# Kernel optimization log

Hardware: AMD Instinct MI355X
Metric: run time of the kernel (lower is better)

The kernel has to match this reference:

```python
import jax, jax.numpy as jnp
import numpy as np

NP, NA = 60000, 30000          # paper / author node counts
EC, EW, EB = 300000, 150000, 150000
IN_F, HID, H, D, NCLS = 1024, 512, 4, 128, 153  # HID = H*D


def setup_inputs() -> dict:
    key = jax.random.key(0)
    ks = jax.random.split(key, 24)
    inp = {
        "x_paper": jax.random.normal(ks[0], (NP, IN_F), jnp.float32),
        "x_author": jax.random.normal(ks[1], (NA, IN_F), jnp.float32),
        "cites_src": jax.random.randint(ks[2], (EC,), 0, NP, jnp.int32),
        "cites_dst": jax.random.randint(ks[3], (EC,), 0, NP, jnp.int32),
        "writes_src": jax.random.randint(ks[4], (EW,), 0, NA, jnp.int32),
        "writes_dst": jax.random.randint(ks[5], (EW,), 0, NP, jnp.int32),
        "wb_src": jax.random.randint(ks[6], (EB,), 0, NP, jnp.int32),
        "wb_dst": jax.random.randint(ks[7], (EB,), 0, NA, jnp.int32),
        "W0": jax.random.normal(ks[8], (3, IN_F, HID), jnp.float32) * 0.02,
        "al0": jax.random.normal(ks[9], (3, H, D), jnp.float32) * 0.1,
        "ar0": jax.random.normal(ks[10], (3, H, D), jnp.float32) * 0.1,
        "W1": jax.random.normal(ks[11], (3, HID, HID), jnp.float32) * 0.03,
        "al1": jax.random.normal(ks[12], (3, H, D), jnp.float32) * 0.1,
        "ar1": jax.random.normal(ks[13], (3, H, D), jnp.float32) * 0.1,
        "W2": jax.random.normal(ks[14], (3, HID, HID), jnp.float32) * 0.03,
        "al2": jax.random.normal(ks[15], (3, H, D), jnp.float32) * 0.1,
        "ar2": jax.random.normal(ks[16], (3, H, D), jnp.float32) * 0.1,
        "linW": jax.random.normal(ks[17], (HID, NCLS), jnp.float32) * 0.02,
        "linb": jnp.zeros((NCLS,), jnp.float32),
    }
    return inp


def gat_conv(h_src, h_dst, src, dst, W, al, ar, n_dst):
    """DGL-style GATConv on one edge type (bipartite block, shared fc)."""
    zs = (h_src @ W).reshape(-1, H, D)            # (Ns,H,D)
    zd = (h_dst @ W).reshape(-1, H, D)            # (Nd,H,D)
    el = jnp.sum(zs * al, axis=-1)                # (Ns,H)
    er = jnp.sum(zd * ar, axis=-1)                # (Nd,H)
    e = jax.nn.leaky_relu(el[src] + er[dst], 0.2)  # (E,H)
    # edge softmax over incoming edges per destination node
    m = jax.ops.segment_max(e, dst, num_segments=n_dst)
    m = jnp.where(jnp.isfinite(m), m, 0.0)
    ee = jnp.exp(e - m[dst])
    s = jax.ops.segment_sum(ee, dst, num_segments=n_dst)
    a = ee / (s[dst] + 1e-9)                      # (E,H)
    # weighted message aggregation: (Nd,H,D)
    return jax.ops.segment_sum(a[:, :, None] * zs[src], dst, num_segments=n_dst)


def reference(x_paper, x_author, cites_src, cites_dst, writes_src, writes_dst,
              wb_src, wb_dst, W0, al0, ar0, W1, al1, ar1, W2, al2, ar2,
              linW, linb):
    def hetero_layer(hp, ha, W, al, ar, act):
        # HeteroGraphConv: sum-aggregate per destination node type
        op = (gat_conv(hp, hp, cites_src, cites_dst, W[0], al[0], ar[0], NP)
              + gat_conv(ha, hp, writes_src, writes_dst, W[1], al[1], ar[1], NP))
        oa = gat_conv(hp, ha, wb_src, wb_dst, W[2], al[2], ar[2], NA)
        op = op.reshape(NP, H * D)   # head-flatten as in forward()
        oa = oa.reshape(NA, H * D)
        if act:
            op, oa = jax.nn.relu(op), jax.nn.relu(oa)
        return op, oa

    hp, ha = x_paper, x_author
    hp, ha = hetero_layer(hp, ha, W0, al0, ar0, True)
    hp, ha = hetero_layer(hp, ha, W1, al1, ar1, True)
    hp, ha = hetero_layer(hp, ha, W2, al2, ar2, False)  # last layer: no activation
    return hp @ linW + linb
```

## Files before the change

kernel.cpp:

```cpp
#include <hip/hip_runtime.h>
#include <cstddef>
#include <cstdint>

static constexpr int NP = 60000, NA = 30000;
static constexpr int EC = 300000, EW = 150000, EB = 150000;
static constexpr int IN_F = 1024, HID = 512, H = 4, D = 128, NCLS = 153;
static constexpr int MPAD_P = 60032;
static constexpr int MPAD_A = 30080;

typedef __attribute__((ext_vector_type(8))) short short8;
typedef __attribute__((ext_vector_type(4))) float float4v;

__device__ __forceinline__ unsigned short f2bf(float f) {
    unsigned int u = __float_as_uint(f);
    unsigned int r = u + 0x7FFFu + ((u >> 16) & 1u);
    return (unsigned short)(r >> 16);
}
__device__ __forceinline__ float bf2f(unsigned short h) {
    return __uint_as_float(((unsigned int)h) << 16);
}

__device__ __forceinline__ void gll16(const unsigned short* g, unsigned short* l) {
    __builtin_amdgcn_global_load_lds(
        (const __attribute__((address_space(1))) unsigned int*)g,
        (__attribute__((address_space(3))) unsigned int*)l, 16, 0, 0);
}

__global__ void hist_kernel(const int* __restrict__ dst, int E, int* __restrict__ counts) {
    int e = blockIdx.x * 256 + threadIdx.x;
    if (e < E) atomicAdd(&counts[dst[e]], 1);
}

__global__ void exscan_kernel(const int* __restrict__ in, int* __restrict__ out, int n) {
    __shared__ int wsum[4];
    int t = threadIdx.x;
    int lane = t & 63, w = t >> 6;
    int carry = 0;
    const int CH = 256 * 8;
    for (int base = 0; base < n; base += CH) {
        int v[8], run[8];
        int i0 = base + t * 8;
        int tsum = 0;
#pragma unroll
        for (int j = 0; j < 8; ++j) {
            int i = i0 + j;
            v[j] = (i < n) ? in[i] : 0;
            tsum += v[j];
            run[j] = tsum;
        }
        int x = tsum;
#pragma unroll
        for (int off = 1; off < 64; off <<= 1) {
            int y = __shfl_up(x, off);
            if (lane >= off) x += y;
        }
        if (lane == 63) wsum[w] = x;
        __syncthreads();
        int wpre = 0;
        for (int ww = 0; ww < w; ++ww) wpre += wsum[ww];
        int chunktot = wsum[0] + wsum[1] + wsum[2] + wsum[3];
        int pre = carry + wpre + (x - tsum);
#pragma unroll
        for (int j = 0; j < 8; ++j) {
            int i = i0 + j;
            if (i < n) out[i] = pre + run[j] - v[j];
        }
        carry += chunktot;
        __syncthreads();
    }
    if (t == 0) out[n] = carry;
}

__global__ void fill_kernel(const int* __restrict__ src, const int* __restrict__ dst, int E,
                            int* __restrict__ cursor, int* __restrict__ col) {
    int e = blockIdx.x * 256 + threadIdx.x;
    if (e < E) {
        int pos = atomicAdd(&cursor[dst[e]], 1);
        col[pos] = src[e];
    }
}

__global__ void decomp4_kernel(const float4* __restrict__ x, ushort4* __restrict__ hi,
                               ushort4* __restrict__ lo, int M, int K, int Mpad) {
    size_t i4 = (size_t)blockIdx.x * 256 + threadIdx.x;
    size_t tot = ((size_t)Mpad * K) >> 2;
    if (i4 >= tot) return;
    size_t row = (i4 * 4) / (size_t)K;
    float4 v = make_float4(0.f, 0.f, 0.f, 0.f);
    if (row < (size_t)M) v = x[i4];
    ushort4 h, l;
    h.x = f2bf(v.x); h.y = f2bf(v.y); h.z = f2bf(v.z); h.w = f2bf(v.w);
    l.x = f2bf(v.x - bf2f(h.x)); l.y = f2bf(v.y - bf2f(h.y));
    l.z = f2bf(v.z - bf2f(h.z)); l.w = f2bf(v.w - bf2f(h.w));
    hi[i4] = h; lo[i4] = l;
}

__global__ void btprep_kernel(const float* __restrict__ W, unsigned short* __restrict__ hi,
                              unsigned short* __restrict__ lo, int K, int N, int Npad) {
    int i = blockIdx.x * 256 + threadIdx.x;
    if (i >= Npad * K) return;
    int n = i / K, k = i - n * K;
    float v = (n < N) ? W[(size_t)k * N + n] : 0.f;
    unsigned short h = f2bf(v);
    hi[i] = h;
    lo[i] = f2bf(v - bf2f(h));
}

__global__ __launch_bounds__(256, 2) void gemm_mfma3(
    const unsigned short* __restrict__ Ahi, const unsigned short* __restrict__ Alo,
    const unsigned short* __restrict__ Bhi, const unsigned short* __restrict__ Blo,
    const float* __restrict__ bias, float* __restrict__ C,
    int M, int K, int Nstore, int ldc) {
    __shared__ unsigned short Ash[128 * 32];
    __shared__ unsigned short Asl[128 * 32];
    __shared__ unsigned short Bsh[256 * 32];
    __shared__ unsigned short Bsl[256 * 32];
    int tid = threadIdx.x;
    int lane = tid & 63, w = tid >> 6;
    int wr = w >> 1, wc = w & 1;
    int bm = blockIdx.y * 128, bn = blockIdx.x * 256;
    int sr = lane >> 2;
    int sc = (lane & 3) * 8;

    float4v acc[4][8];
    float4v zf = {0.f, 0.f, 0.f, 0.f};
#pragma unroll
    for (int i = 0; i < 4; ++i)
#pragma unroll
        for (int j = 0; j < 8; ++j) acc[i][j] = zf;

    int arow = wr * 64 + (lane & 15);
    int brow = wc * 128 + (lane & 15);
    int koff = (lane >> 4) * 8;

    for (int kk = 0; kk < K; kk += 32) {
        size_t a0 = (size_t)(bm + w * 16 + sr) * K + kk + sc;
        size_t a1 = (size_t)(bm + (w + 4) * 16 + sr) * K + kk + sc;
        gll16(Ahi + a0, &Ash[w * 512]);
        gll16(Ahi + a1, &Ash[(w + 4) * 512]);
        gll16(Alo + a0, &Asl[w * 512]);
        gll16(Alo + a1, &Asl[(w + 4) * 512]);
#pragma unroll
        for (int c = 0; c < 4; ++c) {
            size_t b0 = (size_t)(bn + (w + 4 * c) * 16 + sr) * K + kk + sc;
            gll16(Bhi + b0, &Bsh[(w + 4 * c) * 512]);
            gll16(Blo + b0, &Bsl[(w + 4 * c) * 512]);
        }
        __syncthreads();
        short8 fa[4], fb[8], fl[4];
#pragma unroll
        for (int i = 0; i < 4; ++i)
            fa[i] = *(const short8*)&Ash[(arow + i * 16) * 32 + koff];
#pragma unroll
        for (int j = 0; j < 8; ++j)
            fb[j] = *(const short8*)&Bsh[(brow + j * 16) * 32 + koff];
#pragma unroll
        for (int i = 0; i < 4; ++i)
#pragma unroll
            for (int j = 0; j < 8; ++j)
                acc[i][j] = __builtin_amdgcn_mfma_f32_16x16x32_bf16(fa[i], fb[j], acc[i][j], 0, 0, 0);
#pragma unroll
        for (int i = 0; i < 4; ++i)
            fl[i] = *(const short8*)&Asl[(arow + i * 16) * 32 + koff];
#pragma unroll
        for (int i = 0; i < 4; ++i)
#pragma unroll
            for (int j = 0; j < 8; ++j)
                acc[i][j] = __builtin_amdgcn_mfma_f32_16x16x32_bf16(fl[i], fb[j], acc[i][j], 0, 0, 0);
#pragma unroll
        for (int j = 0; j < 8; ++j)
            fb[j] = *(const short8*)&Bsl[(brow + j * 16) * 32 + koff];
#pragma unroll
        for (int i = 0; i < 4; ++i)
#pragma unroll
            for (int j = 0; j < 8; ++j)
                acc[i][j] = __builtin_amdgcn_mfma_f32_16x16x32_bf16(fa[i], fb[j], acc[i][j], 0, 0, 0);
        __syncthreads();
    }
    int col0 = bn + wc * 128 + (lane & 15);
    int row00 = bm + wr * 64 + (lane >> 4) * 4;
#pragma unroll
    for (int i = 0; i < 4; ++i) {
#pragma unroll
        for (int j = 0; j < 8; ++j) {
            int col = col0 + j * 16;
            if (col >= Nstore) continue;
            float badd = bias ? bias[col] : 0.f;
            int rowb = row00 + i * 16;
#pragma unroll
            for (int r = 0; r < 4; ++r) {
                int row = rowb + r;
                if (row < M) C[(size_t)row * ldc + col] = acc[i][j][r] + badd;
            }
        }
    }
}

__global__ __launch_bounds__(256) void eler_kernel(
    const float* __restrict__ z, const float* __restrict__ al, const float* __restrict__ ar,
    float* __restrict__ el, float* __restrict__ er, int M) {
    int row = blockIdx.x * 4 + (threadIdx.x >> 6);
    int lane = threadIdx.x & 63;
    if (row >= M) return;
    const float4* zr = (const float4*)(z + (size_t)row * 512 + lane * 8);
    float4 z0 = zr[0], z1 = zr[1];
    const float4* alp = (const float4*)(al + lane * 8);
    float4 a0 = alp[0], a1 = alp[1];
    float s = z0.x * a0.x + z0.y * a0.y + z0.z * a0.z + z0.w * a0.w
            + z1.x * a1.x + z1.y * a1.y + z1.z * a1.z + z1.w * a1.w;
    s += __shfl_xor(s, 8); s += __shfl_xor(s, 4); s += __shfl_xor(s, 2); s += __shfl_xor(s, 1);
    int h = lane >> 4;
    if ((lane & 15) == 0) el[(size_t)row * 4 + h] = s;
    if (er) {
        const float4* arp = (const float4*)(ar + lane * 8);
        float4 b0 = arp[0], b1 = arp[1];
        float t = z0.x * b0.x + z0.y * b0.y + z0.z * b0.z + z0.w * b0.w
                + z1.x * b1.x + z1.y * b1.y + z1.z * b1.z + z1.w * b1.w;
        t += __shfl_xor(t, 8); t += __shfl_xor(t, 4); t += __shfl_xor(t, 2); t += __shfl_xor(t, 1);
        if ((lane & 15) == 0) er[(size_t)row * 4 + h] = t;
    }
}

__global__ void fold_kernel(const float* __restrict__ W, const float* __restrict__ ar,
                            float* __restrict__ v, int K) {
    int i = blockIdx.x * 256 + threadIdx.x;
    if (i >= K * 4) return;
    int k = i >> 2, h = i & 3;
    const float* wr = W + (size_t)k * 512 + h * 128;
    const float* a = ar + h * 128;
    float s = 0.f;
#pragma unroll 4
    for (int d = 0; d < 128; ++d) s += wr[d] * a[d];
    v[i] = s;
}

__global__ __launch_bounds__(256) void skinny_kernel(
    const float* __restrict__ h, const float* __restrict__ v,
    float* __restrict__ er, int M, int K) {
    __shared__ float vs[4096];
    for (int i = threadIdx.x; i < K * 4; i += 256) vs[i] = v[i];
    __syncthreads();
    int row = blockIdx.x * 4 + (threadIdx.x >> 6);
    int lane = threadIdx.x & 63;
    if (row >= M) return;
    const float* hr = h + (size_t)row * K;
    float a0 = 0, a1 = 0, a2 = 0, a3 = 0;
    for (int k = lane; k < K; k += 64) {
        float x = hr[k];
        float4 vv = *(const float4*)&vs[k * 4];
        a0 += x * vv.x; a1 += x * vv.y; a2 += x * vv.z; a3 += x * vv.w;
    }
#pragma unroll
    for (int off = 32; off; off >>= 1) {
        a0 += __shfl_xor(a0, off); a1 += __shfl_xor(a1, off);
        a2 += __shfl_xor(a2, off); a3 += __shfl_xor(a3, off);
    }
    if (lane == 0) *(float4*)&er[(size_t)row * 4] = make_float4(a0, a1, a2, a3);
}

__global__ __launch_bounds__(256) void agg_fused(
    const int* __restrict__ rp1, const int* __restrict__ col1, const float* __restrict__ z1,
    const float* __restrict__ el1, const float* __restrict__ er1,
    const int* __restrict__ rp2, const int* __restrict__ col2, const float* __restrict__ z2,
    const float* __restrict__ el2, const float* __restrict__ er2,
    float* __restrict__ out, unsigned short* __restrict__ hi, unsigned short* __restrict__ lo,
    int N, int do_relu) {
    int j = blockIdx.x * 4 + (threadIdx.x >> 6);
    int lane = threadIdx.x & 63;
    if (j >= N) return;
    int h = lane >> 4;
    float4 acc0 = make_float4(0, 0, 0, 0), acc1 = make_float4(0, 0, 0, 0);

    {
        int e0 = rp1[j], e1 = rp1[j + 1];
        float erh = er1[(size_t)j * 4 + h];
        float m = -INFINITY, s = 0.f;
        for (int e = e0; e < e1; ++e) {
            float x = el1[(size_t)col1[e] * 4 + h] + erh;
            x = (x >= 0.f) ? x : 0.2f * x;
            float mn = fmaxf(m, x);
            s = s * expf(m - mn) + expf(x - mn);
            m = mn;
        }
        float inv = 1.0f / (s + 1e-9f);
        for (int e = e0; e < e1; ++e) {
            int src = col1[e];
            float x = el1[(size_t)src * 4 + h] + erh;
            x = (x >= 0.f) ? x : 0.2f * x;
            float wgt = expf(x - m) * inv;
            const float4* zr = (const float4*)(z1 + (size_t)src * 512 + lane * 8);
            float4 za = zr[0], zb = zr[1];
            acc0.x += wgt * za.x; acc0.y += wgt * za.y; acc0.z += wgt * za.z; acc0.w += wgt * za.w;
            acc1.x += wgt * zb.x; acc1.y += wgt * zb.y; acc1.z += wgt * zb.z; acc1.w += wgt * zb.w;
        }
    }
    if (rp2) {
        int e0 = rp2[j], e1 = rp2[j + 1];
        float erh = er2[(size_t)j * 4 + h];
        float m = -INFINITY, s = 0.f;
        for (int e = e0; e < e1; ++e) {
            float x = el2[(size_t)col2[e] * 4 + h] + erh;
            x = (x >= 0.f) ? x : 0.2f * x;
            float mn = fmaxf(m, x);
            s = s * expf(m - mn) + expf(x - mn);
            m = mn;
        }
        float inv = 1.0f / (s + 1e-9f);
        for (int e = e0; e < e1; ++e) {
            int src = col2[e];
            float x = el2[(size_t)src * 4 + h] + erh;
            x = (x >= 0.f) ? x : 0.2f * x;
            float wgt = expf(x - m) * inv;
            const float4* zr = (const float4*)(z2 + (size_t)src * 512 + lane * 8);
            float4 za = zr[0], zb = zr[1];
            acc0.x += wgt * za.x; acc0.y += wgt * za.y; acc0.z += wgt * za.z; acc0.w += wgt * za.w;
            acc1.x += wgt * zb.x; acc1.y += wgt * zb.y; acc1.z += wgt * zb.z; acc1.w += wgt * zb.w;
        }
    }
    if (do_relu) {
        acc0.x = fmaxf(acc0.x, 0.f); acc0.y = fmaxf(acc0.y, 0.f);
        acc0.z = fmaxf(acc0.z, 0.f); acc0.w = fmaxf(acc0.w, 0.f);
        acc1.x = fmaxf(acc1.x, 0.f); acc1.y = fmaxf(acc1.y, 0.f);
        acc1.z = fmaxf(acc1.z, 0.f); acc1.w = fmaxf(acc1.w, 0.f);
    }
    float* op = out + (size_t)j * 512 + lane * 8;
    *(float4*)op = acc0;
    *(float4*)(op + 4) = acc1;
    if (hi) {
        size_t base = (size_t)j * 512 + lane * 8;
        ushort4 h0, h1, l0, l1;
        h0.x = f2bf(acc0.x); h0.y = f2bf(acc0.y); h0.z = f2bf(acc0.z); h0.w = f2bf(acc0.w);
        h1.x = f2bf(acc1.x); h1.y = f2bf(acc1.y); h1.z = f2bf(acc1.z); h1.w = f2bf(acc1.w);
        l0.x = f2bf(acc0.x - bf2f(h0.x)); l0.y = f2bf(acc0.y - bf2f(h0.y));
        l0.z = f2bf(acc0.z - bf2f(h0.z)); l0.w = f2bf(acc0.w - bf2f(h0.w));
        l1.x = f2bf(acc1.x - bf2f(h1.x)); l1.y = f2bf(acc1.y - bf2f(h1.y));
        l1.z = f2bf(acc1.z - bf2f(h1.z)); l1.w = f2bf(acc1.w - bf2f(h1.w));
        *(ushort4*)(hi + base) = h0;
        *(ushort4*)(hi + base + 4) = h1;
        *(ushort4*)(lo + base) = l0;
        *(ushort4*)(lo + base + 4) = l1;
    }
}

extern "C" void kernel_launch(void* const* d_in, const int* in_sizes, int n_in,
                              void* d_out, int out_size, void* d_ws, size_t ws_size,
                              hipStream_t stream) {
    const float* x_paper = (const float*)d_in[0];
    const float* x_author = (const float*)d_in[1];
    const int* cites_src = (const int*)d_in[2];
    const int* cites_dst = (const int*)d_in[3];
    const int* writes_src = (const int*)d_in[4];
    const int* writes_dst = (const int*)d_in[5];
    const int* wb_src = (const int*)d_in[6];
    const int* wb_dst = (const int*)d_in[7];
    const float* W0 = (const float*)d_in[8];
    const float* al0 = (const float*)d_in[9];
    const float* ar0 = (const float*)d_in[10];
    const float* W1 = (const float*)d_in[11];
    const float* al1 = (const float*)d_in[12];
    const float* ar1 = (const float*)d_in[13];
    const float* W2 = (const float*)d_in[14];
    const float* al2 = (const float*)d_in[15];
    const float* ar2 = (const float*)d_in[16];
    const float* linW = (const float*)d_in[17];
    const float* linb = (const float*)d_in[18];
    float* out = (float*)d_out;

    char* p = (char*)d_ws;
    auto alloc = [&](size_t n) { char* r = p; p += (n + 255) & ~(size_t)255; return r; };

    float* hpA = (float*)alloc((size_t)NP * 512 * 4);
    float* hpB = (float*)alloc((size_t)NP * 512 * 4);
    float* haA = (float*)alloc((size_t)NA * 512 * 4);
    float* haB = (float*)alloc((size_t)NA * 512 * 4);
    float* zbuf = (float*)alloc((size_t)NP * 512 * 4);
    float* elA = (float*)alloc((size_t)NP * 16);
    float* erA = (float*)alloc((size_t)NP * 16);
    float* elB = (float*)alloc((size_t)NP * 16);
    float* erB = (float*)alloc((size_t)NP * 16);
    float* vfold = (float*)alloc(4096 * 4);
    int* rp_c = (int*)alloc((NP + 1) * 4);
    int* col_c = (int*)alloc((size_t)EC * 4);
    int* rp_w = (int*)alloc((NP + 1) * 4);
    int* col_w = (int*)alloc((size_t)EW * 4);
    int* rp_b = (int*)alloc((NA + 1) * 4);
    int* col_b = (int*)alloc((size_t)EB * 4);
    int* cursor = (int*)alloc((NP + 1) * 4);
    int* counts = (int*)alloc((size_t)NP * 4);

    unsigned short* AhiP = (unsigned short*)alloc((size_t)MPAD_P * 1024 * 2);
    unsigned short* AloP = (unsigned short*)alloc((size_t)MPAD_P * 1024 * 2);
    unsigned short* AhiA = (unsigned short*)alloc((size_t)MPAD_A * 1024 * 2);
    unsigned short* AloA = (unsigned short*)alloc((size_t)MPAD_A * 1024 * 2);
    const int Ks[3] = {IN_F, HID, HID};
    unsigned short *bthi[3][3], *btlo[3][3];
    for (int l = 0; l < 3; ++l)
        for (int t = 0; t < 3; ++t) {
            bthi[l][t] = (unsigned short*)alloc((size_t)512 * Ks[l] * 2);
            btlo[l][t] = (unsigned short*)alloc((size_t)512 * Ks[l] * 2);
        }
    unsigned short* btLhi = (unsigned short*)alloc((size_t)256 * 512 * 2);
    unsigned short* btLlo = (unsigned short*)alloc((size_t)256 * 512 * 2);
    (void)ws_size;

    struct EdgeT { const int* src; const int* dst; int E; int n; int* rp; int* col; };
    EdgeT ets[3] = {
        {cites_src, cites_dst, EC, NP, rp_c, col_c},
        {writes_src, writes_dst, EW, NP, rp_w, col_w},
        {wb_src, wb_dst, EB, NA, rp_b, col_b},
    };
    for (int t = 0; t < 3; ++t) {
        hipMemsetAsync(counts, 0, (size_t)ets[t].n * 4, stream);
        hist_kernel<<<(ets[t].E + 255) / 256, 256, 0, stream>>>(ets[t].dst, ets[t].E, counts);
        exscan_kernel<<<1, 256, 0, stream>>>(counts, ets[t].rp, ets[t].n);
        hipMemcpyAsync(cursor, ets[t].rp, (size_t)ets[t].n * 4, hipMemcpyDeviceToDevice, stream);
        fill_kernel<<<(ets[t].E + 255) / 256, 256, 0, stream>>>(ets[t].src, ets[t].dst, ets[t].E, cursor, ets[t].col);
    }

    const float* Wl[3] = {W0, W1, W2};
    const float* alL[3] = {al0, al1, al2};
    const float* arL[3] = {ar0, ar1, ar2};

    for (int l = 0; l < 3; ++l) {
        int K = Ks[l];
        for (int t = 0; t < 3; ++t)
            btprep_kernel<<<(512 * K + 255) / 256, 256, 0, stream>>>(
                Wl[l] + (size_t)t * K * 512, bthi[l][t], btlo[l][t], K, 512, 512);
    }
    btprep_kernel<<<(256 * 512 + 255) / 256, 256, 0, stream>>>(linW, btLhi, btLlo, 512, NCLS, 256);

    decomp4_kernel<<<((size_t)MPAD_P * 1024 / 4 + 255) / 256, 256, 0, stream>>>(
        (const float4*)x_paper, (ushort4*)AhiP, (ushort4*)AloP, NP, 1024, MPAD_P);
    decomp4_kernel<<<((size_t)MPAD_A * 1024 / 4 + 255) / 256, 256, 0, stream>>>(
        (const float4*)x_author, (ushort4*)AhiA, (ushort4*)AloA, NA, 1024, MPAD_A);

    auto gemm = [&](const unsigned short* Ah, const unsigned short* Al,
                    const unsigned short* Bh, const unsigned short* Bl,
                    const float* bias, float* C, int M, int Mpad, int K, int gx,
                    int Nstore, int ldc) {
        dim3 g(gx, Mpad / 128);
        gemm_mfma3<<<g, 256, 0, stream>>>(Ah, Al, Bh, Bl, bias, C, M, K, Nstore, ldc);
    };

    const float* hp = x_paper;
    const float* ha = x_author;
    for (int l = 0; l < 3; ++l) {
        int K = Ks[l];
        float* hp_n = (l & 1) ? hpB : hpA;
        float* ha_n = (l & 1) ? haB : haA;
        float* zbuf_w = ha_n;
        const float* W = Wl[l];
        const float* al = alL[l];
        const float* ar = arL[l];
        size_t wstride = (size_t)K * 512;
        int relu = (l < 2) ? 1 : 0;

        gemm(AhiP, AloP, bthi[l][0], btlo[l][0], nullptr, zbuf, NP, MPAD_P, K, 2, 512, 512);
        gemm(AhiA, AloA, bthi[l][1], btlo[l][1], nullptr, zbuf_w, NA, MPAD_A, K, 2, 512, 512);
        eler_kernel<<<(NP + 3) / 4, 256, 0, stream>>>(zbuf, al, ar, elA, erA, NP);
        eler_kernel<<<(NA + 3) / 4, 256, 0, stream>>>(zbuf_w, al + 512, nullptr, elB, nullptr, NA);
        fold_kernel<<<(K * 4 + 255) / 256, 256, 0, stream>>>(W + wstride, ar + 512, vfold, K);
        skinny_kernel<<<(NP + 3) / 4, 256, 0, stream>>>(hp, vfold, erB, NP, K);
        agg_fused<<<(NP + 3) / 4, 256, 0, stream>>>(
            rp_c, col_c, zbuf, elA, erA,
            rp_w, col_w, zbuf_w, elB, erB,
            hp_n, nullptr, nullptr, NP, relu);
        gemm(AhiP, AloP, bthi[l][2], btlo[l][2], nullptr, zbuf, NP, MPAD_P, K, 2, 512, 512);
        decomp4_kernel<<<((size_t)MPAD_P * 512 / 4 + 255) / 256, 256, 0, stream>>>(
            (const float4*)hp_n, (ushort4*)AhiP, (ushort4*)AloP, NP, 512, MPAD_P);
        eler_kernel<<<(NP + 3) / 4, 256, 0, stream>>>(zbuf, al + 1024, nullptr, elA, nullptr, NP);
        fold_kernel<<<(K * 4 + 255) / 256, 256, 0, stream>>>(W + 2 * wstride, ar + 1024, vfold, K);
        skinny_kernel<<<(NA + 3) / 4, 256, 0, stream>>>(ha, vfold, erA, NA, K);
        agg_fused<<<(NA + 3) / 4, 256, 0, stream>>>(
            rp_b, col_b, zbuf, elA, erA,
            nullptr, nullptr, nullptr, nullptr, nullptr,
            ha_n, (l < 2) ? AhiA : nullptr, (l < 2) ? AloA : nullptr, NA, relu);
        hp = hp_n;
        ha = ha_n;
    }
    gemm(AhiP, AloP, btLhi, btLlo, linb, out, NP, MPAD_P, 512, 1, NCLS, NCLS);
}
```

Measured before the change: 3.373 ms.

## Replace split-bf16 GEMM with 256x256 tile, 4-stage LDS ring pipeline

The split-bf16 GEMM moves to a 512-thread block with a 256x256 output tile. Each of the three hi/lo product passes becomes its own stage in a 4-slot LDS ring (128KB dynamic shared memory). Global-to-LDS loads are prefetched three stages ahead and gated by vmcnt waits and raw barriers, with an XOR swizzle to cut LDS bank conflicts and setprio around the MFMA bursts. The aim is to overlap memory loads with MFMA and raise arithmetic intensity per block. In exchange it needs larger M padding, far more LDS per block (which limits occupancy), and correctness depends on the hand-counted waitcnt values.

```diff
diff --git a/kernel.cpp b/kernel.cpp
--- a/kernel.cpp
+++ b/kernel.cpp
@@ -5,8 +5,8 @@
 static constexpr int NP = 60000, NA = 30000;
 static constexpr int EC = 300000, EW = 150000, EB = 150000;
 static constexpr int IN_F = 1024, HID = 512, H = 4, D = 128, NCLS = 153;
-static constexpr int MPAD_P = 60032;
-static constexpr int MPAD_A = 30080;
+static constexpr int MPAD_P = 60160;
+static constexpr int MPAD_A = 30208;
 
 typedef __attribute__((ext_vector_type(8))) short short8;
 typedef __attribute__((ext_vector_type(4))) float float4v;
@@ -106,91 +106,128 @@
     lo[i] = f2bf(v - bf2f(h));
 }
 
-__global__ __launch_bounds__(256, 2) void gemm_mfma3(
+__global__ __launch_bounds__(512, 2) void gemm_ring(
     const unsigned short* __restrict__ Ahi, const unsigned short* __restrict__ Alo,
     const unsigned short* __restrict__ Bhi, const unsigned short* __restrict__ Blo,
     const float* __restrict__ bias, float* __restrict__ C,
     int M, int K, int Nstore, int ldc) {
-    __shared__ unsigned short Ash[128 * 32];
-    __shared__ unsigned short Asl[128 * 32];
-    __shared__ unsigned short Bsh[256 * 32];
-    __shared__ unsigned short Bsl[256 * 32];
-    int tid = threadIdx.x;
-    int lane = tid & 63, w = tid >> 6;
-    int wr = w >> 1, wc = w & 1;
-    int bm = blockIdx.y * 128, bn = blockIdx.x * 256;
-    int sr = lane >> 2;
-    int sc = (lane & 3) * 8;
-
-    float4v acc[4][8];
+    extern __shared__ unsigned short lds[];
+    const int tid = threadIdx.x;
+    const int lane = tid & 63;
+    const int w = tid >> 6;
+    const int wr = w >> 2, wc = w & 3;
+    const int bm = blockIdx.y * 256, bn = blockIdx.x * 256;
+
+    const int st_row = w * 16 + (lane >> 2);
+    const int st_sc = (((lane & 3) ^ ((lane >> 3) & 3)) << 3);
+    const size_t aoff0 = (size_t)(bm + st_row) * K + st_sc;
+    const size_t aoff1 = aoff0 + (size_t)128 * K;
+    const size_t boff0 = (size_t)(bn + st_row) * K + st_sc;
+    const size_t boff1 = boff0 + (size_t)128 * K;
+    const int ldsA = w * 512;
+    const int ldsB = 8192 + w * 512;
+
+    const int arow = wr * 128 + (lane & 15);
+    const int brow = wc * 64 + (lane & 15);
+    const int rq = ((((lane >> 4) & 3) ^ ((lane >> 1) & 3)) << 3);
+    const int aRead = arow * 32 + rq;
+    const int bRead = 8192 + brow * 32 + rq;
+
+    float4v acc[8][4];
     float4v zf = {0.f, 0.f, 0.f, 0.f};
 #pragma unroll
-    for (int i = 0; i < 4; ++i)
-#pragma unroll
-        for (int j = 0; j < 8; ++j) acc[i][j] = zf;
-
-    int arow = wr * 64 + (lane & 15);
-    int brow = wc * 128 + (lane & 15);
-    int koff = (lane >> 4) * 8;
-
-    for (int kk = 0; kk < K; kk += 32) {
-        size_t a0 = (size_t)(bm + w * 16 + sr) * K + kk + sc;
-        size_t a1 = (size_t)(bm + (w + 4) * 16 + sr) * K + kk + sc;
-        gll16(Ahi + a0, &Ash[w * 512]);
-        gll16(Ahi + a1, &Ash[(w + 4) * 512]);
-        gll16(Alo + a0, &Asl[w * 512]);
-        gll16(Alo + a1, &Asl[(w + 4) * 512]);
-#pragma unroll
-        for (int c = 0; c < 4; ++c) {
-            size_t b0 = (size_t)(bn + (w + 4 * c) * 16 + sr) * K + kk + sc;
-            gll16(Bhi + b0, &Bsh[(w + 4 * c) * 512]);
-            gll16(Blo + b0, &Bsl[(w + 4 * c) * 512]);
-        }
-        __syncthreads();
-        short8 fa[4], fb[8], fl[4];
-#pragma unroll
-        for (int i = 0; i < 4; ++i)
-            fa[i] = *(const short8*)&Ash[(arow + i * 16) * 32 + koff];
-#pragma unroll
-        for (int j = 0; j < 8; ++j)
-            fb[j] = *(const short8*)&Bsh[(brow + j * 16) * 32 + koff];
-#pragma unroll
-        for (int i = 0; i < 4; ++i)
-#pragma unroll
-            for (int j = 0; j < 8; ++j)
+    for (int i = 0; i < 8; ++i)
+#pragma unroll
+        for (int j = 0; j < 4; ++j) acc[i][j] = zf;
+
+    auto STAGE = [&](unsigned rr, const unsigned short* As, const unsigned short* Bs, int kc) {
+        unsigned short* sb = &lds[rr * 16384u];
+        gll16(As + aoff0 + kc, sb + ldsA);
+        gll16(As + aoff1 + kc, sb + ldsA + 4096);
+        gll16(Bs + boff0 + kc, sb + ldsB);
+        gll16(Bs + boff1 + kc, sb + ldsB + 4096);
+    };
+    auto COMPUTE = [&](unsigned rr) {
+        const unsigned short* sb = &lds[rr * 16384u];
+        short8 fa[8], fb[4];
+#pragma unroll
+        for (int i = 0; i < 8; ++i) fa[i] = *(const short8*)&sb[aRead + i * 512];
+#pragma unroll
+        for (int j = 0; j < 4; ++j) fb[j] = *(const short8*)&sb[bRead + j * 512];
+        __builtin_amdgcn_s_setprio(1);
+#pragma unroll
+        for (int i = 0; i < 8; ++i)
+#pragma unroll
+            for (int j = 0; j < 4; ++j)
                 acc[i][j] = __builtin_amdgcn_mfma_f32_16x16x32_bf16(fa[i], fb[j], acc[i][j], 0, 0, 0);
-#pragma unroll
-        for (int i = 0; i < 4; ++i)
-            fl[i] = *(const short8*)&Asl[(arow + i * 16) * 32 + koff];
-#pragma unroll
-        for (int i = 0; i < 4; ++i)
-#pragma unroll
-            for (int j = 0; j < 8; ++j)
-                acc[i][j] = __builtin_amdgcn_mfma_f32_16x16x32_bf16(fl[i], fb[j], acc[i][j], 0, 0, 0);
-#pragma unroll
-        for (int j = 0; j < 8; ++j)
-            fb[j] = *(const short8*)&Bsl[(brow + j * 16) * 32 + koff];
-#pragma unroll
-        for (int i = 0; i < 4; ++i)
-#pragma unroll
-            for (int j = 0; j < 8; ++j)
-                acc[i][j] = __builtin_amdgcn_mfma_f32_16x16x32_bf16(fa[i], fb[j], acc[i][j], 0, 0, 0);
-        __syncthreads();
-    }
-    int col0 = bn + wc * 128 + (lane & 15);
-    int row00 = bm + wr * 64 + (lane >> 4) * 4;
-#pragma unroll
-    for (int i = 0; i < 4; ++i) {
-#pragma unroll
-        for (int j = 0; j < 8; ++j) {
+        __builtin_amdgcn_s_setprio(0);
+    };
+
+#define WAITV(n) asm volatile("s_waitcnt vmcnt(" #n ")" ::: "memory")
+#define BARF()                                 \
+    do {                                       \
+        asm volatile("" ::: "memory");         \
+        __builtin_amdgcn_s_barrier();          \
+        asm volatile("" ::: "memory");         \
+    } while (0)
+
+    STAGE(0, Ahi, Bhi, 0);
+    STAGE(1, Alo, Bhi, 0);
+    STAGE(2, Ahi, Blo, 0);
+    unsigned rg = 0;
+    const int nK = K >> 5;
+#pragma unroll 1
+    for (int t3 = 0; t3 < nK - 1; ++t3) {
+        const int kn = (t3 + 1) << 5;
+        STAGE((rg + 3) & 3, Ahi, Bhi, kn);
+        WAITV(12);
+        BARF();
+        COMPUTE(rg);
+        BARF();
+        rg = (rg + 1) & 3;
+        STAGE((rg + 3) & 3, Alo, Bhi, kn);
+        WAITV(12);
+        BARF();
+        COMPUTE(rg);
+        BARF();
+        rg = (rg + 1) & 3;
+        STAGE((rg + 3) & 3, Ahi, Blo, kn);
+        WAITV(12);
+        BARF();
+        COMPUTE(rg);
+        BARF();
+        rg = (rg + 1) & 3;
+    }
+    WAITV(8);
+    BARF();
+    COMPUTE(rg);
+    BARF();
+    rg = (rg + 1) & 3;
+    WAITV(4);
+    BARF();
+    COMPUTE(rg);
+    BARF();
+    rg = (rg + 1) & 3;
+    WAITV(0);
+    BARF();
+    COMPUTE(rg);
+#undef WAITV
+#undef BARF
+
+    const int col0 = bn + wc * 64 + (lane & 15);
+    const int row0 = bm + wr * 128 + ((lane >> 4) << 2);
+#pragma unroll
+    for (int i = 0; i < 8; ++i) {
+#pragma unroll
+        for (int j = 0; j < 4; ++j) {
             int col = col0 + j * 16;
             if (col >= Nstore) continue;
             float badd = bias ? bias[col] : 0.f;
-            int rowb = row00 + i * 16;
-#pragma unroll
-            for (int r = 0; r < 4; ++r) {
-                int row = rowb + r;
-                if (row < M) C[(size_t)row * ldc + col] = acc[i][j][r] + badd;
+            int rowb = row0 + i * 16;
+#pragma unroll
+            for (int k = 0; k < 4; ++k) {
+                int row = rowb + k;
+                if (row < M) C[(size_t)row * ldc + col] = acc[i][j][k] + badd;
             }
         }
     }
@@ -366,6 +403,9 @@
     const float* linb = (const float*)d_in[18];
     float* out = (float*)d_out;
 
+    (void)hipFuncSetAttribute((const void*)gemm_ring,
+                              hipFuncAttributeMaxDynamicSharedMemorySize, 131072);
+
     char* p = (char*)d_ws;
     auto alloc = [&](size_t n) { char* r = p; p += (n + 255) & ~(size_t)255; return r; };
 
@@ -438,8 +478,8 @@
                     const unsigned short* Bh, const unsigned short* Bl,
                     const float* bias, float* C, int M, int Mpad, int K, int gx,
                     int Nstore, int ldc) {
-        dim3 g(gx, Mpad / 128);
-        gemm_mfma3<<<g, 256, 0, stream>>>(Ah, Al, Bh, Bl, bias, C, M, K, Nstore, ldc);
+        dim3 g(gx, Mpad / 256);
+        gemm_ring<<<g, 512, 131072, stream>>>(Ah, Al, Bh, Bl, bias, C, M, K, Nstore, ldc);
     };
 
     const float* hp = x_paper;
```

After: 3.377 ms. About the same (+0.1%).

## Restructure split-bf16 GEMM with double-buffered LDS A tiles and direct B register loads

Applied to the files above, without the earlier changes.

Replaces the 128x256 split-bf16 GEMM with a 128x128 tile kernel. It double-buffers the A hi/lo tiles in LDS with an XOR swizzle and prefetches the next K-slice, and it loads the B hi/lo fragments straight from global memory into registers instead of staging them in LDS. It also adds s_setprio around the MFMA bursts and raises the launch-bounds occupancy hint to 3 blocks. Grid widths double to match the smaller tile. The aim is to overlap global loads with MFMA work, cut LDS traffic and bank conflicts, and raise occupancy; the cost is redundant uncoalesced B reads from global/L2 and one fewer barrier per iteration.

```diff
diff --git a/kernel.cpp b/kernel.cpp
--- a/kernel.cpp
+++ b/kernel.cpp
@@ -106,91 +106,106 @@
     lo[i] = f2bf(v - bf2f(h));
 }
 
-__global__ __launch_bounds__(256, 2) void gemm_mfma3(
+__global__ __launch_bounds__(256, 3) void gemm_bd(
     const unsigned short* __restrict__ Ahi, const unsigned short* __restrict__ Alo,
     const unsigned short* __restrict__ Bhi, const unsigned short* __restrict__ Blo,
     const float* __restrict__ bias, float* __restrict__ C,
     int M, int K, int Nstore, int ldc) {
-    __shared__ unsigned short Ash[128 * 32];
-    __shared__ unsigned short Asl[128 * 32];
-    __shared__ unsigned short Bsh[256 * 32];
-    __shared__ unsigned short Bsl[256 * 32];
-    int tid = threadIdx.x;
-    int lane = tid & 63, w = tid >> 6;
-    int wr = w >> 1, wc = w & 1;
-    int bm = blockIdx.y * 128, bn = blockIdx.x * 256;
-    int sr = lane >> 2;
-    int sc = (lane & 3) * 8;
-
-    float4v acc[4][8];
+    __shared__ unsigned short lds[2][8192];
+    const int tid = threadIdx.x;
+    const int lane = tid & 63;
+    const int w = tid >> 6;
+    const int wr = w >> 1, wc = w & 1;
+    const int bm = blockIdx.y * 128, bn = blockIdx.x * 128;
+
+    const int st_row = w * 32 + (lane >> 2);
+    const int st_sc = (((lane & 3) ^ ((lane >> 3) & 3)) << 3);
+    const size_t aoff0 = (size_t)(bm + st_row) * K + st_sc;
+    const size_t aoff1 = aoff0 + (size_t)16 * K;
+    const int ldsW = w * 1024;
+
+    const int arow = wr * 64 + (lane & 15);
+    const int rq = ((((lane >> 4) & 3) ^ ((lane >> 1) & 3)) << 3);
+    const int aRd = arow * 32 + rq;
+
+    const size_t bbase = (size_t)(bn + wc * 64 + (lane & 15)) * K + ((lane >> 4) << 3);
+    const unsigned short* bh = Bhi + bbase;
+    const unsigned short* bl = Blo + bbase;
+    const size_t bjs = (size_t)16 * K;
+
+    float4v acc[4][4];
     float4v zf = {0.f, 0.f, 0.f, 0.f};
 #pragma unroll
     for (int i = 0; i < 4; ++i)
 #pragma unroll
-        for (int j = 0; j < 8; ++j) acc[i][j] = zf;
-
-    int arow = wr * 64 + (lane & 15);
-    int brow = wc * 128 + (lane & 15);
-    int koff = (lane >> 4) * 8;
-
-    for (int kk = 0; kk < K; kk += 32) {
-        size_t a0 = (size_t)(bm + w * 16 + sr) * K + kk + sc;
-        size_t a1 = (size_t)(bm + (w + 4) * 16 + sr) * K + kk + sc;
-        gll16(Ahi + a0, &Ash[w * 512]);
-        gll16(Ahi + a1, &Ash[(w + 4) * 512]);
-        gll16(Alo + a0, &Asl[w * 512]);
-        gll16(Alo + a1, &Asl[(w + 4) * 512]);
-#pragma unroll
-        for (int c = 0; c < 4; ++c) {
-            size_t b0 = (size_t)(bn + (w + 4 * c) * 16 + sr) * K + kk + sc;
-            gll16(Bhi + b0, &Bsh[(w + 4 * c) * 512]);
-            gll16(Blo + b0, &Bsl[(w + 4 * c) * 512]);
-        }
+        for (int j = 0; j < 4; ++j) acc[i][j] = zf;
+
+#define MF(a, b, c) __builtin_amdgcn_mfma_f32_16x16x32_bf16(a, b, c, 0, 0, 0)
+
+    gll16(Ahi + aoff0, &lds[0][ldsW]);
+    gll16(Ahi + aoff1, &lds[0][ldsW + 512]);
+    gll16(Alo + aoff0, &lds[0][4096 + ldsW]);
+    gll16(Alo + aoff1, &lds[0][4096 + ldsW + 512]);
+
+    const int nK = K >> 5;
+#pragma unroll 1
+    for (int c = 0; c < nK; ++c) {
         __syncthreads();
-        short8 fa[4], fb[8], fl[4];
+        const int kk = c << 5;
+        if (c + 1 < nK) {
+            unsigned short* d = &lds[(c + 1) & 1][0];
+            gll16(Ahi + aoff0 + kk + 32, d + ldsW);
+            gll16(Ahi + aoff1 + kk + 32, d + ldsW + 512);
+            gll16(Alo + aoff0 + kk + 32, d + 4096 + ldsW);
+            gll16(Alo + aoff1 + kk + 32, d + 4096 + ldsW + 512);
+        }
+        const unsigned short* s = &lds[c & 1][0];
+        short8 fbhi[4], fblo[4];
+#pragma unroll
+        for (int j = 0; j < 4; ++j) fbhi[j] = *(const short8*)(bh + j * bjs + kk);
+#pragma unroll
+        for (int j = 0; j < 4; ++j) fblo[j] = *(const short8*)(bl + j * bjs + kk);
+        short8 fahi[4], falo[4];
+#pragma unroll
+        for (int i = 0; i < 4; ++i) fahi[i] = *(const short8*)&s[aRd + i * 512];
+        __builtin_amdgcn_s_setprio(1);
 #pragma unroll
         for (int i = 0; i < 4; ++i)
-            fa[i] = *(const short8*)&Ash[(arow + i * 16) * 32 + koff];
-#pragma unroll
-        for (int j = 0; j < 8; ++j)
-            fb[j] = *(const short8*)&Bsh[(brow + j * 16) * 32 + koff];
+#pragma unroll
+            for (int j = 0; j < 4; ++j)
+                acc[i][j] = MF(fahi[i], fbhi[j], acc[i][j]);
+        __builtin_amdgcn_s_setprio(0);
+#pragma unroll
+        for (int i = 0; i < 4; ++i) falo[i] = *(const short8*)&s[4096 + aRd + i * 512];
+        __builtin_amdgcn_s_setprio(1);
 #pragma unroll
         for (int i = 0; i < 4; ++i)
 #pragma unroll
-            for (int j = 0; j < 8; ++j)
-                acc[i][j] = __builtin_amdgcn_mfma_f32_16x16x32_bf16(fa[i], fb[j], acc[i][j], 0, 0, 0);
+            for (int j = 0; j < 4; ++j)
+                acc[i][j] = MF(falo[i], fbhi[j], acc[i][j]);
 #pragma unroll
         for (int i = 0; i < 4; ++i)
-            fl[i] = *(const short8*)&Asl[(arow + i * 16) * 32 + koff];
-#pragma unroll
-        for (int i = 0; i < 4; ++i)
-#pragma unroll
-            for (int j = 0; j < 8; ++j)
-                acc[i][j] = __builtin_amdgcn_mfma_f32_16x16x32_bf16(fl[i], fb[j], acc[i][j], 0, 0, 0);
-#pragma unroll
-        for (int j = 0; j < 8; ++j)
-            fb[j] = *(const short8*)&Bsl[(brow + j * 16) * 32 + koff];
-#pragma unroll
-        for (int i = 0; i < 4; ++i)
-#pragma unroll
-            for (int j = 0; j < 8; ++j)
-                acc[i][j] = __builtin_amdgcn_mfma_f32_16x16x32_bf16(fa[i], fb[j], acc[i][j], 0, 0, 0);
-        __syncthreads();
-    }
-    int col0 = bn + wc * 128 + (lane & 15);
-    int row00 = bm + wr * 64 + (lane >> 4) * 4;
+#pragma unroll
+            for (int j = 0; j < 4; ++j)
+                acc[i][j] = MF(fahi[i], fblo[j], acc[i][j]);
+        __builtin_amdgcn_s_setprio(0);
+    }
+#undef MF
+
+    const int col0 = bn + wc * 64 + (lane & 15);
+    const int row0 = bm + wr * 64 + ((lane >> 4) << 2);
 #pragma unroll
     for (int i = 0; i < 4; ++i) {
 #pragma unroll
-        for (int j = 0; j < 8; ++j) {
+        for (int j = 0; j < 4; ++j) {
             int col = col0 + j * 16;
             if (col >= Nstore) continue;
             float badd = bias ? bias[col] : 0.f;
-            int rowb = row00 + i * 16;
-#pragma unroll
-            for (int r = 0; r < 4; ++r) {
-                int row = rowb + r;
-                if (row < M) C[(size_t)row * ldc + col] = acc[i][j][r] + badd;
+            int rowb = row0 + i * 16;
+#pragma unroll
+            for (int k = 0; k < 4; ++k) {
+                int row = rowb + k;
+                if (row < M) C[(size_t)row * ldc + col] = acc[i][j][k] + badd;
             }
         }
     }
@@ -439,7 +454,7 @@
                     const float* bias, float* C, int M, int Mpad, int K, int gx,
                     int Nstore, int ldc) {
         dim3 g(gx, Mpad / 128);
-        gemm_mfma3<<<g, 256, 0, stream>>>(Ah, Al, Bh, Bl, bias, C, M, K, Nstore, ldc);
+        gemm_bd<<<g, 256, 0, stream>>>(Ah, Al, Bh, Bl, bias, C, M, K, Nstore, ldc);
     };
 
     const float* hp = x_paper;
@@ -455,8 +470,8 @@
         size_t wstride = (size_t)K * 512;
         int relu = (l < 2) ? 1 : 0;
 
-        gemm(AhiP, AloP, bthi[l][0], btlo[l][0], nullptr, zbuf, NP, MPAD_P, K, 2, 512, 512);
-        gemm(AhiA, AloA, bthi[l][1], btlo[l][1], nullptr, zbuf_w, NA, MPAD_A, K, 2, 512, 512);
+        gemm(AhiP, AloP, bthi[l][0], btlo[l][0], nullptr, zbuf, NP, MPAD_P, K, 4, 512, 512);
+        gemm(AhiA, AloA, bthi[l][1], btlo[l][1], nullptr, zbuf_w, NA, MPAD_A, K, 4, 512, 512);
         eler_kernel<<<(NP + 3) / 4, 256, 0, stream>>>(zbuf, al, ar, elA, erA, NP);
         eler_kernel<<<(NA + 3) / 4, 256, 0, stream>>>(zbuf_w, al + 512, nullptr, elB, nullptr, NA);
         fold_kernel<<<(K * 4 + 255) / 256, 256, 0, stream>>>(W + wstride, ar + 512, vfold, K);
@@ -465,7 +480,7 @@
             rp_c, col_c, zbuf, elA, erA,
             rp_w, col_w, zbuf_w, elB, erB,
             hp_n, nullptr, nullptr, NP, relu);
-        gemm(AhiP, AloP, bthi[l][2], btlo[l][2], nullptr, zbuf, NP, MPAD_P, K, 2, 512, 512);
+        gemm(AhiP, AloP, bthi[l][2], btlo[l][2], nullptr, zbuf, NP, MPAD_P, K, 4, 512, 512);
         decomp4_kernel<<<((size_t)MPAD_P * 512 / 4 + 255) / 256, 256, 0, stream>>>(
             (const float4*)hp_n, (ushort4*)AhiP, (ushort4*)AloP, NP, 512, MPAD_P);
         eler_kernel<<<(NP + 3) / 4, 256, 0, stream>>>(zbuf, al + 1024, nullptr, elA, nullptr, NP);
@@ -478,5 +493,5 @@
         hp = hp_n;
         ha = ha_n;
     }
-    gemm(AhiP, AloP, btLhi, btLlo, linb, out, NP, MPAD_P, 512, 1, NCLS, NCLS);
-}
+    gemm(AhiP, AloP, btLhi, btLlo, linb, out, NP, MPAD_P, 512, 2, NCLS, NCLS);
+}
```

Measured after the change: 4.105 ms. +21.7%, slower.
